# Performance work log

Hardware: AMD Instinct MI355X
Metric: run time of the kernel (lower is better)

The kernel has to match this reference:

```python
import jax, jax.numpy as jnp
import numpy as np


def _pointnet(x, w1, b1, w2, b2, w3, b3):
    # x: [B, P, 5] -> pointwise MLP then max-pool over points -> [B, 64]
    h = jax.nn.relu(x @ w1.T + b1)
    h = jax.nn.relu(h @ w2.T + b2)
    h = h @ w3.T + b3
    return h.max(axis=1)


def _lstm_layer(x, wih, whh, bih, bhh):
    # x: [B, T, D]; PyTorch gate order i, f, g, o
    B = x.shape[0]
    H = whh.shape[1]
    def step(carry, xt):
        h, c = carry
        g = xt @ wih.T + bih + h @ whh.T + bhh
        i, f, gg, o = jnp.split(g, 4, axis=-1)
        c = jax.nn.sigmoid(f) * c + jax.nn.sigmoid(i) * jnp.tanh(gg)
        h = jax.nn.sigmoid(o) * jnp.tanh(c)
        return (h, c), h
    init = (jnp.zeros((B, H), x.dtype), jnp.zeros((B, H), x.dtype))
    (h_last, _), hs = jax.lax.scan(step, init, jnp.swapaxes(x, 0, 1))
    return jnp.swapaxes(hs, 0, 1), h_last


def _edge_conv(h, mask, wt, bt, wp, bp):
    # DGL EdgeConv: h_i' = max_{j in N(i)} theta(h_j - h_i) + phi(h_i)
    # theta is linear -> max_j (Th_j) - Th_i + b_theta + phi(h_i)
    Th = h @ wt.T                       # [V,128]
    Ph = h @ wp.T + bp                  # [V,128]
    neigh_max = jnp.max(jnp.where(mask[:, :, None], Th[None, :, :], -jnp.inf), axis=1)
    return neigh_max - Th + bt + Ph


def _edge_regr(e, w1, b1, w2, b2):
    return jax.nn.sigmoid(jax.nn.relu(e @ w1.T + b1) @ w2.T + b2)


def _affinity(h, N, M, er_w1, er_b1, er_w2, er_b2):
    # faithful to source: edges[i*M+j] = h[j] - h[i]  (j indexes first M rows, as in the code)
    E = (h[None, :M, :] - h[:N, None, :]).reshape(N * M, -1)
    return _edge_regr(E, er_w1, er_b1, er_w2, er_b2).reshape(N, M)


def setup_inputs() -> dict:
    key = jax.random.key(0)
    ks = iter(jax.random.split(key, 40))
    N, M, P, T = 256, 256, 512, 10
    lin = lambda k, o, i: (jax.random.normal(k, (o, i), jnp.float32) / np.sqrt(i)).astype(jnp.float32)
    inp = {
        'det_pts': jax.random.normal(next(ks), (N, P, 5), jnp.float32),
        'det_boxes': jax.random.normal(next(ks), (N, 9), jnp.float32),
        'track_pts': jax.random.normal(next(ks), (M, P, 5), jnp.float32),
        'track_boxes': jax.random.normal(next(ks), (M, T, 9), jnp.float32),
        'adj': jax.random.randint(next(ks), (N + M, N + M), 0, 2, jnp.int32),
        'pn_w1': lin(next(ks), 64, 5), 'pn_b1': jnp.zeros((64,), jnp.float32),
        'pn_w2': lin(next(ks), 128, 64), 'pn_b2': jnp.zeros((128,), jnp.float32),
        'pn_w3': lin(next(ks), 64, 128), 'pn_b3': jnp.zeros((64,), jnp.float32),
        'dm_w1': lin(next(ks), 32, 9), 'dm_b1': jnp.zeros((32,), jnp.float32),
        'dm_w2': lin(next(ks), 64, 32), 'dm_b2': jnp.zeros((64,), jnp.float32),
        'l0_wih': lin(next(ks), 256, 9), 'l0_whh': lin(next(ks), 256, 64),
        'l0_bih': jnp.zeros((256,), jnp.float32), 'l0_bhh': jnp.zeros((256,), jnp.float32),
        'l1_wih': lin(next(ks), 256, 64), 'l1_whh': lin(next(ks), 256, 64),
        'l1_bih': jnp.zeros((256,), jnp.float32), 'l1_bhh': jnp.zeros((256,), jnp.float32),
        'gc_wt': jnp.stack([lin(next(ks), 128, 128) for _ in range(4)]),
        'gc_bt': jnp.zeros((4, 128), jnp.float32),
        'gc_wp': jnp.stack([lin(next(ks), 128, 128) for _ in range(4)]),
        'gc_bp': jnp.zeros((4, 128), jnp.float32),
        'er_w1': lin(next(ks), 64, 128), 'er_b1': jnp.zeros((64,), jnp.float32),
        'er_w2': lin(next(ks), 1, 64), 'er_b2': jnp.zeros((1,), jnp.float32),
    }
    return inp


def reference(det_pts, det_boxes, track_pts, track_boxes, adj,
              pn_w1, pn_b1, pn_w2, pn_b2, pn_w3, pn_b3,
              dm_w1, dm_b1, dm_w2, dm_b2,
              l0_wih, l0_whh, l0_bih, l0_bhh,
              l1_wih, l1_whh, l1_bih, l1_bhh,
              gc_wt, gc_bt, gc_wp, gc_bp,
              er_w1, er_b1, er_w2, er_b2):
    N, M = det_pts.shape[0], track_pts.shape[0]
    V = N + M
    # appearance features (shared PointNet)
    det_app = _pointnet(det_pts, pn_w1, pn_b1, pn_w2, pn_b2, pn_w3, pn_b3)    # [N,64]
    trk_app = _pointnet(track_pts, pn_w1, pn_b1, pn_w2, pn_b2, pn_w3, pn_b3)  # [M,64]
    # motion features
    det_mot = jax.nn.relu(det_boxes @ dm_w1.T + dm_b1) @ dm_w2.T + dm_b2      # [N,64]
    hs0, _ = _lstm_layer(track_boxes, l0_wih, l0_whh, l0_bih, l0_bhh)
    _, trk_mot = _lstm_layer(hs0, l1_wih, l1_whh, l1_bih, l1_bhh)             # [M,64]
    h = jnp.concatenate([
        jnp.concatenate([det_app, det_mot], axis=1),
        jnp.concatenate([trk_app, trk_mot], axis=1)], axis=0)                 # [V,128]
    # neighbor-source mask: edge i->j for adj[i,j]!=0, plus self-loops
    mask = (adj.T != 0) | jnp.eye(V, dtype=bool)                              # mask[i,j]: j is source neighbor of i
    aff1 = None
    for k in range(4):
        h = jax.nn.relu(_edge_conv(h, mask, gc_wt[k], gc_bt[k], gc_wp[k], gc_bp[k]))
        if k == 0:
            aff1 = _affinity(h, N, M, er_w1, er_b1, er_w2, er_b2)
    aff_final = _affinity(h, N, M, er_w1, er_b1, er_w2, er_b2)
    return jnp.stack([aff1, aff_final])  # [2, N, M]
```

## Files before the change

kernel.cpp:

```cpp
#include <hip/hip_runtime.h>
#include <math.h>

#define NDET 256
#define NTRK 256
#define NV   512
#define PPTS 512

typedef short bf16x8 __attribute__((ext_vector_type(8)));
typedef float f32x4  __attribute__((ext_vector_type(4)));

__device__ __forceinline__ float sigf(float x) { return 1.f / (1.f + expf(-x)); }

__device__ __forceinline__ short f2bf(float f) {
    unsigned u = __float_as_uint(f);
    u += 0x7fffu + ((u >> 16) & 1u);
    return (short)(u >> 16);
}
__device__ __forceinline__ unsigned pack2bf(float lo, float hi) {
    return (unsigned)(unsigned short)f2bf(lo) | ((unsigned)(unsigned short)f2bf(hi) << 16);
}

__global__ __launch_bounds__(256) void pointnet_kernel(
    const float* __restrict__ det_pts, const float* __restrict__ track_pts,
    const float* __restrict__ w1, const float* __restrict__ b1,
    const float* __restrict__ w2, const float* __restrict__ b2,
    const float* __restrict__ w3, const float* __restrict__ b3,
    float* __restrict__ hout)
{
    __shared__ __align__(16) short sW2[128][72];
    __shared__ __align__(16) short sW3[64][136];
    __shared__ __align__(16) short sH1[64][72];
    __shared__ __align__(16) short sH2[64][136];
    __shared__ __align__(16) float sX[320];
    __shared__ float sW1f[64][6];
    __shared__ float sB1[64];

    const int t  = threadIdx.x;
    const int b  = blockIdx.x;
    const int w  = t >> 6;
    const int ln = t & 15;
    const int kq = (t >> 4) & 3;
    const float* x = (b < NDET) ? (det_pts + (size_t)b * PPTS * 5)
                                : (track_pts + (size_t)(b - NDET) * PPTS * 5);

    for (int i = t; i < 8192; i += 256) sW2[i >> 6][i & 63] = f2bf(w2[i]);
    for (int i = t; i < 8192; i += 256) sW3[i >> 7][i & 127] = f2bf(w3[i]);
    for (int i = t; i < 320; i += 256) sW1f[i / 5][i % 5] = w1[i];
    if (t < 64) sB1[t] = b1[t];
    __syncthreads();

    bf16x8 bf2[2][2];
#pragma unroll
    for (int nt = 0; nt < 2; ++nt)
#pragma unroll
        for (int Kt = 0; Kt < 2; ++Kt)
            bf2[nt][Kt] = *(const bf16x8*)&sW2[32 * w + 16 * nt + ln][kq * 8 + 32 * Kt];
    bf16x8 bf3[4];
#pragma unroll
    for (int Kt = 0; Kt < 4; ++Kt)
        bf3[Kt] = *(const bf16x8*)&sW3[16 * w + ln][kq * 8 + 32 * Kt];
    float bn[2];
#pragma unroll
    for (int nt = 0; nt < 2; ++nt) bn[nt] = b2[32 * w + 16 * nt + ln];

    float runmax[4] = {-1e30f, -1e30f, -1e30f, -1e30f};

    const int pt = t & 63;
    for (int c = 0; c < PPTS / 64; ++c) {
        for (int i = t; i < 320; i += 256) sX[i] = x[c * 320 + i];
        __syncthreads();

        {
            float xv[5];
#pragma unroll
            for (int k = 0; k < 5; ++k) xv[k] = sX[pt * 5 + k];
#pragma unroll
            for (int jj = 0; jj < 8; ++jj) {
                const int d0 = w * 16 + 2 * jj;
                float a0 = sB1[d0], a1 = sB1[d0 + 1];
#pragma unroll
                for (int k = 0; k < 5; ++k) {
                    a0 = fmaf(xv[k], sW1f[d0][k], a0);
                    a1 = fmaf(xv[k], sW1f[d0 + 1][k], a1);
                }
                *(unsigned*)&sH1[pt][d0] = pack2bf(fmaxf(a0, 0.f), fmaxf(a1, 0.f));
            }
        }
        __syncthreads();

        {
            bf16x8 af[4][2];
#pragma unroll
            for (int Mt = 0; Mt < 4; ++Mt)
#pragma unroll
                for (int Kt = 0; Kt < 2; ++Kt)
                    af[Mt][Kt] = *(const bf16x8*)&sH1[16 * Mt + ln][kq * 8 + 32 * Kt];
#pragma unroll
            for (int Mt = 0; Mt < 4; ++Mt) {
#pragma unroll
                for (int nt = 0; nt < 2; ++nt) {
                    f32x4 cacc = {0.f, 0.f, 0.f, 0.f};
                    cacc = __builtin_amdgcn_mfma_f32_16x16x32_bf16(af[Mt][0], bf2[nt][0], cacc, 0, 0, 0);
                    cacc = __builtin_amdgcn_mfma_f32_16x16x32_bf16(af[Mt][1], bf2[nt][1], cacc, 0, 0, 0);
                    const int col = 32 * w + 16 * nt + ln;
#pragma unroll
                    for (int r = 0; r < 4; ++r)
                        sH2[16 * Mt + kq * 4 + r][col] = f2bf(fmaxf(cacc[r] + bn[nt], 0.f));
                }
            }
        }
        __syncthreads();

        {
#pragma unroll
            for (int Mt = 0; Mt < 4; ++Mt) {
                f32x4 cacc = {0.f, 0.f, 0.f, 0.f};
#pragma unroll
                for (int Kt = 0; Kt < 4; ++Kt) {
                    const bf16x8 a = *(const bf16x8*)&sH2[16 * Mt + ln][kq * 8 + 32 * Kt];
                    cacc = __builtin_amdgcn_mfma_f32_16x16x32_bf16(a, bf3[Kt], cacc, 0, 0, 0);
                }
#pragma unroll
                for (int r = 0; r < 4; ++r) runmax[r] = fmaxf(runmax[r], cacc[r]);
            }
        }
        __syncthreads();
    }

    float rm = fmaxf(fmaxf(runmax[0], runmax[1]), fmaxf(runmax[2], runmax[3]));
    rm = fmaxf(rm, __shfl_xor(rm, 16));
    rm = fmaxf(rm, __shfl_xor(rm, 32));
    if ((t & 63) < 16) {
        const int n = 16 * w + ln;
        hout[b * 128 + n] = rm + b3[n];
    }
}

__global__ __launch_bounds__(64) void detmot_kernel(
    const float* __restrict__ det_boxes,
    const float* __restrict__ w1, const float* __restrict__ b1,
    const float* __restrict__ w2, const float* __restrict__ b2,
    float* __restrict__ hout)
{
    __shared__ float sx[9];
    __shared__ float sh[32];
    const int t = threadIdx.x, d = blockIdx.x;
    if (t < 9) sx[t] = det_boxes[d * 9 + t];
    __syncthreads();
    if (t < 32) {
        float a = b1[t];
#pragma unroll
        for (int k = 0; k < 9; ++k) a = fmaf(w1[t * 9 + k], sx[k], a);
        sh[t] = fmaxf(a, 0.f);
    }
    __syncthreads();
    float a = b2[t];
#pragma unroll
    for (int k = 0; k < 32; ++k) a = fmaf(w2[t * 32 + k], sh[k], a);
    hout[d * 128 + 64 + t] = a;
}

__global__ __launch_bounds__(256, 1) void lstm_kernel(
    const float* __restrict__ track_boxes,
    const float* __restrict__ wih0, const float* __restrict__ whh0,
    const float* __restrict__ bih0, const float* __restrict__ bhh0,
    const float* __restrict__ wih1, const float* __restrict__ whh1,
    const float* __restrict__ bih1, const float* __restrict__ bhh1,
    float* __restrict__ hout)
{
    __shared__ float sx[90];
    __shared__ float sg[256];
    __shared__ __align__(16) float sh0[64];
    __shared__ __align__(16) float sh1[64];

    const int t = threadIdx.x;
    const int m = blockIdx.x;
    const int u = t & 63;

    if (t < 90) sx[t] = track_boxes[m * 90 + t];
    if (t < 64) { sh0[t] = 0.f; sh1[t] = 0.f; }

    float w0[9];
#pragma unroll
    for (int k = 0; k < 9; ++k) w0[k] = wih0[t * 9 + k];
    float4 wr0[16], wi1[16], wr1[16];
    {
        const float4* p0 = (const float4*)(whh0 + t * 64);
        const float4* p1 = (const float4*)(wih1 + t * 64);
        const float4* p2 = (const float4*)(whh1 + t * 64);
#pragma unroll
        for (int k = 0; k < 16; ++k) { wr0[k] = p0[k]; wi1[k] = p1[k]; wr1[k] = p2[k]; }
    }
    const float bias0 = bih0[t] + bhh0[t];
    const float bias1 = bih1[t] + bhh1[t];

    float c0 = 0.f, c1 = 0.f, h1reg = 0.f;
    __syncthreads();

    for (int s = 0; s < 10; ++s) {
        {
            float acc0 = bias0, acc1 = 0.f, acc2 = 0.f, acc3 = 0.f;
#pragma unroll
            for (int k = 0; k < 9; ++k) acc0 = fmaf(w0[k], sx[s * 9 + k], acc0);
            const float4* hv = (const float4*)sh0;
#pragma unroll
            for (int k = 0; k < 16; k += 4) {
                float4 hA = hv[k], hB = hv[k + 1], hC = hv[k + 2], hD = hv[k + 3];
                acc0 = fmaf(wr0[k].x, hA.x, acc0); acc0 = fmaf(wr0[k].y, hA.y, acc0);
                acc0 = fmaf(wr0[k].z, hA.z, acc0); acc0 = fmaf(wr0[k].w, hA.w, acc0);
                acc1 = fmaf(wr0[k+1].x, hB.x, acc1); acc1 = fmaf(wr0[k+1].y, hB.y, acc1);
                acc1 = fmaf(wr0[k+1].z, hB.z, acc1); acc1 = fmaf(wr0[k+1].w, hB.w, acc1);
                acc2 = fmaf(wr0[k+2].x, hC.x, acc2); acc2 = fmaf(wr0[k+2].y, hC.y, acc2);
                acc2 = fmaf(wr0[k+2].z, hC.z, acc2); acc2 = fmaf(wr0[k+2].w, hC.w, acc2);
                acc3 = fmaf(wr0[k+3].x, hD.x, acc3); acc3 = fmaf(wr0[k+3].y, hD.y, acc3);
                acc3 = fmaf(wr0[k+3].z, hD.z, acc3); acc3 = fmaf(wr0[k+3].w, hD.w, acc3);
            }
            sg[t] = (acc0 + acc1) + (acc2 + acc3);
        }
        __syncthreads();
        if (t < 64) {
            const float gi = sg[u], gf = sg[64 + u], gg = sg[128 + u], go = sg[192 + u];
            c0 = sigf(gf) * c0 + sigf(gi) * tanhf(gg);
            sh0[u] = sigf(go) * tanhf(c0);
        }
        __syncthreads();
        {
            float acc0 = bias1, acc1 = 0.f, acc2 = 0.f, acc3 = 0.f;
            const float4* xv = (const float4*)sh0;
            const float4* hv = (const float4*)sh1;
#pragma unroll
            for (int k = 0; k < 16; k += 4) {
                float4 xA = xv[k], xB = xv[k + 1], xC = xv[k + 2], xD = xv[k + 3];
                acc0 = fmaf(wi1[k].x, xA.x, acc0); acc0 = fmaf(wi1[k].y, xA.y, acc0);
                acc0 = fmaf(wi1[k].z, xA.z, acc0); acc0 = fmaf(wi1[k].w, xA.w, acc0);
                acc1 = fmaf(wi1[k+1].x, xB.x, acc1); acc1 = fmaf(wi1[k+1].y, xB.y, acc1);
                acc1 = fmaf(wi1[k+1].z, xB.z, acc1); acc1 = fmaf(wi1[k+1].w, xB.w, acc1);
                acc2 = fmaf(wi1[k+2].x, xC.x, acc2); acc2 = fmaf(wi1[k+2].y, xC.y, acc2);
                acc2 = fmaf(wi1[k+2].z, xC.z, acc2); acc2 = fmaf(wi1[k+2].w, xC.w, acc2);
                acc3 = fmaf(wi1[k+3].x, xD.x, acc3); acc3 = fmaf(wi1[k+3].y, xD.y, acc3);
                acc3 = fmaf(wi1[k+3].z, xD.z, acc3); acc3 = fmaf(wi1[k+3].w, xD.w, acc3);
            }
#pragma unroll
            for (int k = 0; k < 16; k += 4) {
                float4 hA = hv[k], hB = hv[k + 1], hC = hv[k + 2], hD = hv[k + 3];
                acc0 = fmaf(wr1[k].x, hA.x, acc0); acc0 = fmaf(wr1[k].y, hA.y, acc0);
                acc0 = fmaf(wr1[k].z, hA.z, acc0); acc0 = fmaf(wr1[k].w, hA.w, acc0);
                acc1 = fmaf(wr1[k+1].x, hB.x, acc1); acc1 = fmaf(wr1[k+1].y, hB.y, acc1);
                acc1 = fmaf(wr1[k+1].z, hB.z, acc1); acc1 = fmaf(wr1[k+1].w, hB.w, acc1);
                acc2 = fmaf(wr1[k+2].x, hC.x, acc2); acc2 = fmaf(wr1[k+2].y, hC.y, acc2);
                acc2 = fmaf(wr1[k+2].z, hC.z, acc2); acc2 = fmaf(wr1[k+2].w, hC.w, acc2);
                acc3 = fmaf(wr1[k+3].x, hD.x, acc3); acc3 = fmaf(wr1[k+3].y, hD.y, acc3);
                acc3 = fmaf(wr1[k+3].z, hD.z, acc3); acc3 = fmaf(wr1[k+3].w, hD.w, acc3);
            }
            sg[t] = (acc0 + acc1) + (acc2 + acc3);
        }
        __syncthreads();
        if (t < 64) {
            const float gi = sg[u], gf = sg[64 + u], gg = sg[128 + u], go = sg[192 + u];
            c1 = sigf(gf) * c1 + sigf(gi) * tanhf(gg);
            h1reg = sigf(go) * tanhf(c1);
            sh1[u] = h1reg;
        }
        __syncthreads();
    }

    if (t < 64) hout[(size_t)(NDET + m) * 128 + 64 + u] = h1reg;
}

__global__ __launch_bounds__(128) void econv_gemm_kernel(
    const float* __restrict__ hin, const float* __restrict__ wt,
    const float* __restrict__ wp, const float* __restrict__ bp,
    float* __restrict__ Th, float* __restrict__ Ph)
{
    __shared__ __align__(16) float srow[128];
    const int t = threadIdx.x, v = blockIdx.x;
    srow[t] = hin[v * 128 + t];
    __syncthreads();
    const float4* hr = (const float4*)srow;
    const float4* wtr = (const float4*)(wt + t * 128);
    const float4* wpr = (const float4*)(wp + t * 128);
    float aT = 0.f, aP = bp[t];
#pragma unroll 8
    for (int k = 0; k < 32; ++k) {
        const float4 h = hr[k];
        const float4 a = wtr[k];
        aT = fmaf(a.x, h.x, aT); aT = fmaf(a.y, h.y, aT);
        aT = fmaf(a.z, h.z, aT); aT = fmaf(a.w, h.w, aT);
        const float4 b = wpr[k];
        aP = fmaf(b.x, h.x, aP); aP = fmaf(b.y, h.y, aP);
        aP = fmaf(b.z, h.z, aP); aP = fmaf(b.w, h.w, aP);
    }
    Th[v * 128 + t] = aT;
    Ph[v * 128 + t] = aP;
}

__global__ __launch_bounds__(128) void econv_max_kernel(
    const int* __restrict__ adj, const float* __restrict__ Th,
    const float* __restrict__ Ph, const float* __restrict__ bt,
    float* __restrict__ hout)
{
    __shared__ float sneg[NV];
    const int t = threadIdx.x, i = blockIdx.x;
    for (int j = t; j < NV; j += 128)
        sneg[j] = ((adj[j * NV + i] != 0) || (j == i)) ? 0.f : -3e38f;
    __syncthreads();

    const float* __restrict__ thp = Th + t;
    float m = -3e38f;
#pragma unroll 1
    for (int j0 = 0; j0 < NV; j0 += 16) {
        float v[16];
#pragma unroll
        for (int jj = 0; jj < 16; ++jj) v[jj] = thp[(j0 + jj) * 128];
#pragma unroll
        for (int jj = 0; jj < 16; ++jj) m = fmaxf(m, v[jj] + sneg[j0 + jj]);
    }
    hout[i * 128 + t] = fmaxf(m - Th[i * 128 + t] + bt[t] + Ph[i * 128 + t], 0.f);
}

__global__ __launch_bounds__(64) void uproj_kernel(
    const float* __restrict__ hin, const float* __restrict__ w1,
    float* __restrict__ u)
{
    __shared__ __align__(16) float srow[128];
    const int t = threadIdx.x, i = blockIdx.x;
    srow[t] = hin[i * 128 + t];
    srow[t + 64] = hin[i * 128 + 64 + t];
    __syncthreads();
    const float4* hr = (const float4*)srow;
    const float4* wr = (const float4*)(w1 + t * 128);
    float a = 0.f;
#pragma unroll 8
    for (int k = 0; k < 32; ++k) {
        const float4 h = hr[k], w = wr[k];
        a = fmaf(w.x, h.x, a); a = fmaf(w.y, h.y, a);
        a = fmaf(w.z, h.z, a); a = fmaf(w.w, h.w, a);
    }
    u[i * 64 + t] = a;
}

__global__ __launch_bounds__(256) void edge_kernel(
    const float* __restrict__ u, const float* __restrict__ b1,
    const float* __restrict__ w2, const float* __restrict__ b2,
    float* __restrict__ out)
{
    __shared__ float sui[64], sw2[64], sb1[64];
    const int t = threadIdx.x, i = blockIdx.x;
    if (t < 64) { sui[t] = u[i * 64 + t]; sw2[t] = w2[t]; sb1[t] = b1[t]; }
    __syncthreads();
    const float4* ur = (const float4*)(u + t * 64);
    float a = b2[0];
#pragma unroll
    for (int k = 0; k < 16; ++k) {
        const float4 uv = ur[k];
        const int k4 = k * 4;
        a = fmaf(sw2[k4 + 0], fmaxf(uv.x - sui[k4 + 0] + sb1[k4 + 0], 0.f), a);
        a = fmaf(sw2[k4 + 1], fmaxf(uv.y - sui[k4 + 1] + sb1[k4 + 1], 0.f), a);
        a = fmaf(sw2[k4 + 2], fmaxf(uv.z - sui[k4 + 2] + sb1[k4 + 2], 0.f), a);
        a = fmaf(sw2[k4 + 3], fmaxf(uv.w - sui[k4 + 3] + sb1[k4 + 3], 0.f), a);
    }
    out[i * 256 + t] = 1.f / (1.f + expf(-a));
}

extern "C" void kernel_launch(void* const* d_in, const int* in_sizes, int n_in,
                              void* d_out, int out_size, void* d_ws, size_t ws_size,
                              hipStream_t stream)
{
    const float* det_pts     = (const float*)d_in[0];
    const float* det_boxes   = (const float*)d_in[1];
    const float* track_pts   = (const float*)d_in[2];
    const float* track_boxes = (const float*)d_in[3];
    const int*   adj         = (const int*)d_in[4];
    const float* pn_w1 = (const float*)d_in[5],  *pn_b1 = (const float*)d_in[6];
    const float* pn_w2 = (const float*)d_in[7],  *pn_b2 = (const float*)d_in[8];
    const float* pn_w3 = (const float*)d_in[9],  *pn_b3 = (const float*)d_in[10];
    const float* dm_w1 = (const float*)d_in[11], *dm_b1 = (const float*)d_in[12];
    const float* dm_w2 = (const float*)d_in[13], *dm_b2 = (const float*)d_in[14];
    const float* l0_wih = (const float*)d_in[15], *l0_whh = (const float*)d_in[16];
    const float* l0_bih = (const float*)d_in[17], *l0_bhh = (const float*)d_in[18];
    const float* l1_wih = (const float*)d_in[19], *l1_whh = (const float*)d_in[20];
    const float* l1_bih = (const float*)d_in[21], *l1_bhh = (const float*)d_in[22];
    const float* gc_wt = (const float*)d_in[23], *gc_bt = (const float*)d_in[24];
    const float* gc_wp = (const float*)d_in[25], *gc_bp = (const float*)d_in[26];
    const float* er_w1 = (const float*)d_in[27], *er_b1 = (const float*)d_in[28];
    const float* er_w2 = (const float*)d_in[29], *er_b2 = (const float*)d_in[30];
    float* out = (float*)d_out;

    float* hA = (float*)d_ws;
    float* hB = hA + NV * 128;
    float* Th = hB + NV * 128;
    float* Ph = Th + NV * 128;
    float* uu = Ph + NV * 128;

    pointnet_kernel<<<NV, 256, 0, stream>>>(det_pts, track_pts,
        pn_w1, pn_b1, pn_w2, pn_b2, pn_w3, pn_b3, hA);
    detmot_kernel<<<NDET, 64, 0, stream>>>(det_boxes, dm_w1, dm_b1, dm_w2, dm_b2, hA);
    lstm_kernel<<<NTRK, 256, 0, stream>>>(track_boxes,
        l0_wih, l0_whh, l0_bih, l0_bhh, l1_wih, l1_whh, l1_bih, l1_bhh, hA);

    float* hin = hA;
    float* hO  = hB;
    for (int k = 0; k < 4; ++k) {
        econv_gemm_kernel<<<NV, 128, 0, stream>>>(hin,
            gc_wt + (size_t)k * 128 * 128, gc_wp + (size_t)k * 128 * 128,
            gc_bp + (size_t)k * 128, Th, Ph);
        econv_max_kernel<<<NV, 128, 0, stream>>>(adj, Th, Ph,
            gc_bt + (size_t)k * 128, hO);
        float* tmp = hin; hin = hO; hO = tmp;
        if (k == 0) {
            uproj_kernel<<<NDET, 64, 0, stream>>>(hin, er_w1, uu);
            edge_kernel<<<NDET, 256, 0, stream>>>(uu, er_b1, er_w2, er_b2, out);
        }
    }
    uproj_kernel<<<NDET, 64, 0, stream>>>(hin, er_w1, uu);
    edge_kernel<<<NDET, 256, 0, stream>>>(uu, er_b1, er_w2, er_b2, out + NDET * NTRK);
}
```

Measured before the change: 279.0 us.

## Fuse edge-conv max with next-layer projection and affinity u-projection; fold detmot into pointnet

Each edge-conv layer's neighbour max now runs in a kernel that also computes the next layer's Th/Ph projections and, where needed, the affinity u-projection. This removes the separate gemm and uproj launches and the round trip of the intermediate h through global memory. The max loop is reorganised so each thread reads a float4 across four column groups, with a shared-memory reduction at the end. The detection-motion MLP is folded into the tail of pointnet_kernel, removing another launch. The main cost is that the per-row 128x128 projections now run inside the max kernel, which has only 128 threads per block.

New measurement: 246.4 us. 1.13x faster.

```diff
diff --git a/kernel.cpp b/kernel.cpp
--- a/kernel.cpp
+++ b/kernel.cpp
@@ -25,6 +25,9 @@
     const float* __restrict__ w1, const float* __restrict__ b1,
     const float* __restrict__ w2, const float* __restrict__ b2,
     const float* __restrict__ w3, const float* __restrict__ b3,
+    const float* __restrict__ det_boxes,
+    const float* __restrict__ dw1, const float* __restrict__ db1,
+    const float* __restrict__ dw2, const float* __restrict__ db2,
     float* __restrict__ hout)
 {
     __shared__ __align__(16) short sW2[128][72];
@@ -34,6 +37,8 @@
     __shared__ __align__(16) float sX[320];
     __shared__ float sW1f[64][6];
     __shared__ float sB1[64];
+    __shared__ float sbox[9];
+    __shared__ float sh32[32];
 
     const int t  = threadIdx.x;
     const int b  = blockIdx.x;
@@ -134,30 +139,24 @@
         const int n = 16 * w + ln;
         hout[b * 128 + n] = rm + b3[n];
     }
-}
-
-__global__ __launch_bounds__(64) void detmot_kernel(
-    const float* __restrict__ det_boxes,
-    const float* __restrict__ w1, const float* __restrict__ b1,
-    const float* __restrict__ w2, const float* __restrict__ b2,
-    float* __restrict__ hout)
-{
-    __shared__ float sx[9];
-    __shared__ float sh[32];
-    const int t = threadIdx.x, d = blockIdx.x;
-    if (t < 9) sx[t] = det_boxes[d * 9 + t];
-    __syncthreads();
-    if (t < 32) {
-        float a = b1[t];
-#pragma unroll
-        for (int k = 0; k < 9; ++k) a = fmaf(w1[t * 9 + k], sx[k], a);
-        sh[t] = fmaxf(a, 0.f);
-    }
-    __syncthreads();
-    float a = b2[t];
-#pragma unroll
-    for (int k = 0; k < 32; ++k) a = fmaf(w2[t * 32 + k], sh[k], a);
-    hout[d * 128 + 64 + t] = a;
+
+    if (b < NDET) {
+        if (t < 9) sbox[t] = det_boxes[b * 9 + t];
+        __syncthreads();
+        if (t < 32) {
+            float a = db1[t];
+#pragma unroll
+            for (int k = 0; k < 9; ++k) a = fmaf(dw1[t * 9 + k], sbox[k], a);
+            sh32[t] = fmaxf(a, 0.f);
+        }
+        __syncthreads();
+        if (t < 64) {
+            float a = db2[t];
+#pragma unroll
+            for (int k = 0; k < 32; ++k) a = fmaf(dw2[t * 32 + k], sh32[k], a);
+            hout[b * 128 + 64 + t] = a;
+        }
+    }
 }
 
 __global__ __launch_bounds__(256, 1) void lstm_kernel(
@@ -294,49 +293,83 @@
     Ph[v * 128 + t] = aP;
 }
 
-__global__ __launch_bounds__(128) void econv_max_kernel(
+__global__ __launch_bounds__(128) void econv_fused_kernel(
     const int* __restrict__ adj, const float* __restrict__ Th,
     const float* __restrict__ Ph, const float* __restrict__ bt,
-    float* __restrict__ hout)
+    const float* __restrict__ wtn, const float* __restrict__ wpn,
+    const float* __restrict__ bpn,
+    const float* __restrict__ erw1, float* __restrict__ uu,
+    float* __restrict__ Thn, float* __restrict__ Phn)
 {
     __shared__ float sneg[NV];
+    __shared__ __align__(16) float4 sred[4][32];
+    __shared__ __align__(16) float sh[128];
+
     const int t = threadIdx.x, i = blockIdx.x;
+    const int l32 = t & 31, grp = t >> 5;
+
     for (int j = t; j < NV; j += 128)
         sneg[j] = ((adj[j * NV + i] != 0) || (j == i)) ? 0.f : -3e38f;
-    __syncthreads();
-
-    const float* __restrict__ thp = Th + t;
-    float m = -3e38f;
-#pragma unroll 1
-    for (int j0 = 0; j0 < NV; j0 += 16) {
-        float v[16];
-#pragma unroll
-        for (int jj = 0; jj < 16; ++jj) v[jj] = thp[(j0 + jj) * 128];
-#pragma unroll
-        for (int jj = 0; jj < 16; ++jj) m = fmaxf(m, v[jj] + sneg[j0 + jj]);
-    }
-    hout[i * 128 + t] = fmaxf(m - Th[i * 128 + t] + bt[t] + Ph[i * 128 + t], 0.f);
-}
-
-__global__ __launch_bounds__(64) void uproj_kernel(
-    const float* __restrict__ hin, const float* __restrict__ w1,
-    float* __restrict__ u)
-{
-    __shared__ __align__(16) float srow[128];
-    const int t = threadIdx.x, i = blockIdx.x;
-    srow[t] = hin[i * 128 + t];
-    srow[t + 64] = hin[i * 128 + 64 + t];
-    __syncthreads();
-    const float4* hr = (const float4*)srow;
-    const float4* wr = (const float4*)(w1 + t * 128);
-    float a = 0.f;
+
+    const float thi = Th[i * 128 + t];
+    const float phi = Ph[i * 128 + t];
+    const float btv = bt[t];
+    __syncthreads();
+
+    float4 mx = {-3e38f, -3e38f, -3e38f, -3e38f};
+    const float* __restrict__ thp = Th + 4 * l32;
+#pragma unroll 4
+    for (int jb = 0; jb < NV; jb += 16) {
+        float4 v[4];
+#pragma unroll
+        for (int jj = 0; jj < 4; ++jj)
+            v[jj] = *(const float4*)&thp[(size_t)(jb + 4 * jj + grp) * 128];
+#pragma unroll
+        for (int jj = 0; jj < 4; ++jj) {
+            const float s = sneg[jb + 4 * jj + grp];
+            mx.x = fmaxf(mx.x, v[jj].x + s);
+            mx.y = fmaxf(mx.y, v[jj].y + s);
+            mx.z = fmaxf(mx.z, v[jj].z + s);
+            mx.w = fmaxf(mx.w, v[jj].w + s);
+        }
+    }
+    sred[grp][l32] = mx;
+    __syncthreads();
+
+    const float* rf = (const float*)sred;
+    const float m = fmaxf(fmaxf(rf[t], rf[128 + t]), fmaxf(rf[256 + t], rf[384 + t]));
+    sh[t] = fmaxf(m - thi + btv + phi, 0.f);
+    __syncthreads();
+
+    const float4* hr = (const float4*)sh;
+    if (wtn) {
+        const float4* wtr = (const float4*)(wtn + t * 128);
+        const float4* wpr = (const float4*)(wpn + t * 128);
+        float aT = 0.f, aP = bpn[t];
 #pragma unroll 8
-    for (int k = 0; k < 32; ++k) {
-        const float4 h = hr[k], w = wr[k];
-        a = fmaf(w.x, h.x, a); a = fmaf(w.y, h.y, a);
-        a = fmaf(w.z, h.z, a); a = fmaf(w.w, h.w, a);
-    }
-    u[i * 64 + t] = a;
+        for (int k = 0; k < 32; ++k) {
+            const float4 h = hr[k];
+            const float4 a = wtr[k];
+            aT = fmaf(a.x, h.x, aT); aT = fmaf(a.y, h.y, aT);
+            aT = fmaf(a.z, h.z, aT); aT = fmaf(a.w, h.w, aT);
+            const float4 b = wpr[k];
+            aP = fmaf(b.x, h.x, aP); aP = fmaf(b.y, h.y, aP);
+            aP = fmaf(b.z, h.z, aP); aP = fmaf(b.w, h.w, aP);
+        }
+        Thn[i * 128 + t] = aT;
+        Phn[i * 128 + t] = aP;
+    }
+    if (erw1 && i < NDET && t < 64) {
+        const float4* wr = (const float4*)(erw1 + t * 128);
+        float a = 0.f;
+#pragma unroll 8
+        for (int k = 0; k < 32; ++k) {
+            const float4 h = hr[k], wv = wr[k];
+            a = fmaf(wv.x, h.x, a); a = fmaf(wv.y, h.y, a);
+            a = fmaf(wv.z, h.z, a); a = fmaf(wv.w, h.w, a);
+        }
+        uu[i * 64 + t] = a;
+    }
 }
 
 __global__ __launch_bounds__(256) void edge_kernel(
@@ -386,32 +419,33 @@
     const float* er_w2 = (const float*)d_in[29], *er_b2 = (const float*)d_in[30];
     float* out = (float*)d_out;
 
-    float* hA = (float*)d_ws;
-    float* hB = hA + NV * 128;
-    float* Th = hB + NV * 128;
-    float* Ph = Th + NV * 128;
-    float* uu = Ph + NV * 128;
+    float* hA  = (float*)d_ws;
+    float* Th  = hA  + NV * 128;
+    float* Ph  = Th  + NV * 128;
+    float* Th2 = Ph  + NV * 128;
+    float* Ph2 = Th2 + NV * 128;
+    float* uu1 = Ph2 + NV * 128;
+    float* uu2 = uu1 + NDET * 64;
 
     pointnet_kernel<<<NV, 256, 0, stream>>>(det_pts, track_pts,
-        pn_w1, pn_b1, pn_w2, pn_b2, pn_w3, pn_b3, hA);
-    detmot_kernel<<<NDET, 64, 0, stream>>>(det_boxes, dm_w1, dm_b1, dm_w2, dm_b2, hA);
+        pn_w1, pn_b1, pn_w2, pn_b2, pn_w3, pn_b3,
+        det_boxes, dm_w1, dm_b1, dm_w2, dm_b2, hA);
     lstm_kernel<<<NTRK, 256, 0, stream>>>(track_boxes,
         l0_wih, l0_whh, l0_bih, l0_bhh, l1_wih, l1_whh, l1_bih, l1_bhh, hA);
 
-    float* hin = hA;
-    float* hO  = hB;
-    for (int k = 0; k < 4; ++k) {
-        econv_gemm_kernel<<<NV, 128, 0, stream>>>(hin,
-            gc_wt + (size_t)k * 128 * 128, gc_wp + (size_t)k * 128 * 128,
-            gc_bp + (size_t)k * 128, Th, Ph);
-        econv_max_kernel<<<NV, 128, 0, stream>>>(adj, Th, Ph,
-            gc_bt + (size_t)k * 128, hO);
-        float* tmp = hin; hin = hO; hO = tmp;
-        if (k == 0) {
-            uproj_kernel<<<NDET, 64, 0, stream>>>(hin, er_w1, uu);
-            edge_kernel<<<NDET, 256, 0, stream>>>(uu, er_b1, er_w2, er_b2, out);
-        }
-    }
-    uproj_kernel<<<NDET, 64, 0, stream>>>(hin, er_w1, uu);
-    edge_kernel<<<NDET, 256, 0, stream>>>(uu, er_b1, er_w2, er_b2, out + NDET * NTRK);
-}
+    econv_gemm_kernel<<<NV, 128, 0, stream>>>(hA,
+        gc_wt, gc_wp, gc_bp, Th, Ph);
+
+    const size_t WSZ = 128 * 128;
+    econv_fused_kernel<<<NV, 128, 0, stream>>>(adj, Th, Ph, gc_bt,
+        gc_wt + WSZ, gc_wp + WSZ, gc_bp + 128, er_w1, uu1, Th2, Ph2);
+    econv_fused_kernel<<<NV, 128, 0, stream>>>(adj, Th2, Ph2, gc_bt + 128,
+        gc_wt + 2 * WSZ, gc_wp + 2 * WSZ, gc_bp + 256, nullptr, nullptr, Th, Ph);
+    econv_fused_kernel<<<NV, 128, 0, stream>>>(adj, Th, Ph, gc_bt + 256,
+        gc_wt + 3 * WSZ, gc_wp + 3 * WSZ, gc_bp + 384, nullptr, nullptr, Th2, Ph2);
+    econv_fused_kernel<<<NV, 128, 0, stream>>>(adj, Th2, Ph2, gc_bt + 384,
+        nullptr, nullptr, nullptr, er_w1, uu2, nullptr, nullptr);
+
+    edge_kernel<<<NDET, 256, 0, stream>>>(uu1, er_b1, er_w2, er_b2, out);
+    edge_kernel<<<NDET, 256, 0, stream>>>(uu2, er_b1, er_w2, er_b2, out + NDET * NTRK);
+}
```
